# Optimization experiments

Hardware: AMD Instinct MI355X
Metric: run time of the kernel (lower is better)

## Reference

```python
import jax, jax.numpy as jnp
import numpy as np

TAU = 0.95

def _f1_per_position(labels):
    # labels: [B, L] binary relevance. r[b, j] = F1 if the list is truncated at position j+1.
    B, L = labels.shape
    csum = jnp.cumsum(labels, axis=1)                       # [B, L] relevant docs kept at cutoff k=j+1
    k = jnp.arange(1, L + 1, dtype=labels.dtype)            # [L]
    total = jnp.sum(labels, axis=1, keepdims=True)          # [B, 1] total relevant per list
    prec = csum / k
    rec = jnp.where(total > 0, csum / jnp.maximum(total, 1.0), 0.0)
    denom = prec + rec
    return jnp.where(denom > 0, 2.0 * prec * rec / jnp.maximum(denom, 1e-20), 0.0)


def setup_inputs() -> dict:
    key = jax.random.key(0)
    k1, k2 = jax.random.split(key)
    B, L = 8192, 2048
    # output: per-position truncation probabilities in (0, 1); log() is applied in the loss.
    output = jax.random.uniform(k1, (B, L, 1), dtype=jnp.float32, minval=1e-4, maxval=1.0)
    labels = jax.random.randint(k2, (B, L), 0, 2).astype(jnp.float32)
    return {"output": output, "labels": labels}


def reference(output, labels):
    # output: [B, L, 1], labels: [B, L]
    B = output.shape[0]
    r = _f1_per_position(labels)                             # [B, L]
    # q = exp(r/tau) / sum_j exp(r/tau)  ==  softmax(r/tau) along positions
    q = jax.nn.softmax(r / TAU, axis=1)
    log_out = jnp.log(output[..., 0])                        # [B, L]
    return -jnp.sum(log_out * q) / B
```

## Files before the change

kernel.cpp:

```cpp
#include <hip/hip_runtime.h>


constexpr int L   = 2048;
constexpr int TPB = 256;
constexpr int EPL = 32;
constexpr float TAU   = 0.95f;
constexpr float LOG2E = 1.4426950408889634f;
constexpr float LN2   = 0.6931471805599453f;

__global__ __launch_bounds__(TPB) void attncut_row_kernel(
    const float* __restrict__ output,
    const float* __restrict__ labels,
    float* __restrict__ rowloss,
    int B)
{
    const int wave = threadIdx.x >> 6;
    const int lane = threadIdx.x & 63;
    const int row  = blockIdx.x * 4 + wave;

    const size_t base = (size_t)row * L + (size_t)lane * EPL;
    const float4* lab4 = reinterpret_cast<const float4*>(labels + base);
    const float4* out4 = reinterpret_cast<const float4*>(output + base);

    unsigned mask = 0u;
#pragma unroll
    for (int c = 0; c < 8; ++c) {
        float4 a = lab4[c];
        unsigned b0 = (unsigned)a.x, b1 = (unsigned)a.y,
                 b2 = (unsigned)a.z, b3 = (unsigned)a.w;
        mask |= (b0 << (4*c)) | (b1 << (4*c+1)) | (b2 << (4*c+2)) | (b3 << (4*c+3));
    }

    float4 o[8];
#pragma unroll
    for (int c = 0; c < 8; ++c) o[c] = out4[c];

    const float run = (float)__popc(mask);
    float x = run;
#pragma unroll
    for (int d = 1; d < 64; d <<= 1) {
        float n = __shfl_up(x, d, 64);
        if (lane >= d) x += n;
    }
    const float total = __shfl(x, 63, 64);
    const float excl  = x - run;

    const float K2 = (total > 0.f) ? (2.f * LOG2E / TAU) : 0.f;
    const float kbase = (float)(lane * EPL) + total;

    float cf = excl;
    float Z = 0.f, W = 0.f;
    const float* of = reinterpret_cast<const float*>(o);
#pragma unroll
    for (int i = 0; i < EPL; ++i) {
        cf += (float)((mask >> i) & 1u);
        float s = (K2 * cf) * __builtin_amdgcn_rcpf(kbase + (float)(i + 1));
        float e = __builtin_amdgcn_exp2f(s);
        Z += e;
        W = fmaf(__builtin_amdgcn_logf(of[i]), e, W);
    }

#pragma unroll
    for (int d = 32; d; d >>= 1) {
        Z += __shfl_xor(Z, d, 64);
        W += __shfl_xor(W, d, 64);
    }
    if (lane == 0) rowloss[row] = -LN2 * W / Z;
}

__global__ __launch_bounds__(TPB) void attncut_reduce_kernel(
    const float* __restrict__ rowloss, float* __restrict__ out, int B)
{
    const int t = threadIdx.x;
    const float4* r4 = reinterpret_cast<const float4*>(rowloss);
    float s = 0.f;
    for (int i = t; i < B / 4; i += TPB) {
        float4 v = r4[i];
        s += (v.x + v.y) + (v.z + v.w);
    }
#pragma unroll
    for (int d = 32; d; d >>= 1) s += __shfl_xor(s, d, 64);
    __shared__ float ws[4];
    if ((t & 63) == 0) ws[t >> 6] = s;
    __syncthreads();
    if (t == 0) out[0] = (ws[0] + ws[1] + ws[2] + ws[3]) / (float)B;
}

extern "C" void kernel_launch(void* const* d_in, const int* in_sizes, int n_in,
                              void* d_out, int out_size, void* d_ws, size_t ws_size,
                              hipStream_t stream) {
    const float* output = (const float*)d_in[0];
    const float* labels = (const float*)d_in[1];
    const int B = in_sizes[1] / L;

    float* rowloss = (float*)d_ws;

    attncut_row_kernel<<<B / 4, TPB, 0, stream>>>(output, labels, rowloss, B);
    attncut_reduce_kernel<<<1, TPB, 0, stream>>>(rowloss, (float*)d_out, B);
}
```

Before: 31.76 us.

## Interleave row elements across lanes for coalesced float4 loads with packed segmented scan

Changes the per-lane data mapping from 32 contiguous elements per lane to 8 interleaved float4 chunks strided by 64 lanes, so each wave load instruction covers a contiguous 1 KB span and is fully coalesced. Because each lane now owns 8 separate segments, the prefix sum becomes 8 separate scans, packed two 16-bit counts per 32-bit word so only 4 shuffle scans are needed. The output loads are also moved into the compute loop instead of being buffered up front. The cost is more shuffle traffic and integer bookkeeping per lane.

```diff
diff --git a/kernel.cpp b/kernel.cpp
--- a/kernel.cpp
+++ b/kernel.cpp
@@ -3,7 +3,6 @@
 
 constexpr int L   = 2048;
 constexpr int TPB = 256;
-constexpr int EPL = 32;
 constexpr float TAU   = 0.95f;
 constexpr float LOG2E = 1.4426950408889634f;
 constexpr float LN2   = 0.6931471805599453f;
@@ -18,54 +17,84 @@
     const int lane = threadIdx.x & 63;
     const int row  = blockIdx.x * 4 + wave;
 
-    const size_t base = (size_t)row * L + (size_t)lane * EPL;
-    const float4* lab4 = reinterpret_cast<const float4*>(labels + base);
-    const float4* out4 = reinterpret_cast<const float4*>(output + base);
+    const float4* lab4 = reinterpret_cast<const float4*>(labels + (size_t)row * L) + lane;
+    const float4* out4 = reinterpret_cast<const float4*>(output + (size_t)row * L) + lane;
 
-    unsigned mask = 0u;
+    unsigned nibs = 0u;
 #pragma unroll
     for (int c = 0; c < 8; ++c) {
-        float4 a = lab4[c];
-        unsigned b0 = (unsigned)a.x, b1 = (unsigned)a.y,
-                 b2 = (unsigned)a.z, b3 = (unsigned)a.w;
-        mask |= (b0 << (4*c)) | (b1 << (4*c+1)) | (b2 << (4*c+2)) | (b3 << (4*c+3));
+        float4 a = lab4[c * 64];
+        unsigned b = (unsigned)a.x | ((unsigned)a.y << 1)
+                   | ((unsigned)a.z << 2) | ((unsigned)a.w << 3);
+        nibs |= b << (4 * c);
     }
 
-    float4 o[8];
+    unsigned w[4];
 #pragma unroll
-    for (int c = 0; c < 8; ++c) o[c] = out4[c];
+    for (int q = 0; q < 4; ++q) {
+        unsigned c0 = __popc((nibs >> (8 * q)) & 0xFu);
+        unsigned c1 = __popc((nibs >> (8 * q + 4)) & 0xFu);
+        w[q] = c0 | (c1 << 16);
+    }
 
-    const float run = (float)__popc(mask);
-    float x = run;
 #pragma unroll
     for (int d = 1; d < 64; d <<= 1) {
-        float n = __shfl_up(x, d, 64);
-        if (lane >= d) x += n;
+#pragma unroll
+        for (int q = 0; q < 4; ++q) {
+            unsigned n = __shfl_up(w[q], d, 64);
+            if (lane >= d) w[q] += n;
+        }
     }
-    const float total = __shfl(x, 63, 64);
-    const float excl  = x - run;
+
+    float T[8], E[8];
+#pragma unroll
+    for (int q = 0; q < 4; ++q) {
+        unsigned tw = __shfl(w[q], 63, 64);
+        unsigned own0 = __popc((nibs >> (8 * q)) & 0xFu);
+        unsigned own1 = __popc((nibs >> (8 * q + 4)) & 0xFu);
+        T[2 * q]     = (float)(tw & 0xFFFFu);
+        T[2 * q + 1] = (float)(tw >> 16);
+        E[2 * q]     = (float)((w[q] & 0xFFFFu) - own0);
+        E[2 * q + 1] = (float)((w[q] >> 16) - own1);
+    }
+    const float total = ((T[0] + T[1]) + (T[2] + T[3])) + ((T[4] + T[5]) + (T[6] + T[7]));
 
     const float K2 = (total > 0.f) ? (2.f * LOG2E / TAU) : 0.f;
-    const float kbase = (float)(lane * EPL) + total;
 
-    float cf = excl;
-    float Z = 0.f, W = 0.f;
-    const float* of = reinterpret_cast<const float*>(o);
+    float Z = 0.f, Wd = 0.f;
+    float off = 0.f;
 #pragma unroll
-    for (int i = 0; i < EPL; ++i) {
-        cf += (float)((mask >> i) & 1u);
-        float s = (K2 * cf) * __builtin_amdgcn_rcpf(kbase + (float)(i + 1));
-        float e = __builtin_amdgcn_exp2f(s);
-        Z += e;
-        W = fmaf(__builtin_amdgcn_logf(of[i]), e, W);
+    for (int c = 0; c < 8; ++c) {
+        float4 ov = out4[c * 64];
+        float cf = off + E[c];
+        const unsigned nib = (nibs >> (4 * c)) & 0xFu;
+        const float kb = total + (float)(c * 256 + 4 * lane);
+
+        cf += (float)(nib & 1u);
+        float e0 = __builtin_amdgcn_exp2f((K2 * cf) * __builtin_amdgcn_rcpf(kb + 1.f));
+        Z += e0;  Wd = fmaf(__builtin_amdgcn_logf(ov.x), e0, Wd);
+
+        cf += (float)((nib >> 1) & 1u);
+        float e1 = __builtin_amdgcn_exp2f((K2 * cf) * __builtin_amdgcn_rcpf(kb + 2.f));
+        Z += e1;  Wd = fmaf(__builtin_amdgcn_logf(ov.y), e1, Wd);
+
+        cf += (float)((nib >> 2) & 1u);
+        float e2 = __builtin_amdgcn_exp2f((K2 * cf) * __builtin_amdgcn_rcpf(kb + 3.f));
+        Z += e2;  Wd = fmaf(__builtin_amdgcn_logf(ov.z), e2, Wd);
+
+        cf += (float)((nib >> 3) & 1u);
+        float e3 = __builtin_amdgcn_exp2f((K2 * cf) * __builtin_amdgcn_rcpf(kb + 4.f));
+        Z += e3;  Wd = fmaf(__builtin_amdgcn_logf(ov.w), e3, Wd);
+
+        off += T[c];
     }
 
 #pragma unroll
     for (int d = 32; d; d >>= 1) {
-        Z += __shfl_xor(Z, d, 64);
-        W += __shfl_xor(W, d, 64);
+        Z  += __shfl_xor(Z, d, 64);
+        Wd += __shfl_xor(Wd, d, 64);
     }
-    if (lane == 0) rowloss[row] = -LN2 * W / Z;
+    if (lane == 0) rowloss[row] = -LN2 * Wd / Z;
 }
 
 __global__ __launch_bounds__(TPB) void attncut_reduce_kernel(
```

Result: faster. 28.69 us (-9.7%).
